# Kernel tuning notes

Hardware: AMD Instinct MI355X
Metric: run time of the kernel (lower is better)

## Reference

```python
import jax, jax.numpy as jnp
import numpy as np

H = 512
W = 512
NSH = 4
MU_BORDER = 1.05
S_MIN = 1.0 / 30.0   # 1 / n_gaussian_max_pixels
S_MAX = 1.0 / 0.75   # 1 / n_gaussian_min_pixels
B = 8192
N = 2048


def setup_inputs() -> dict:
    key = jax.random.key(0)
    k1, k2, k3, k4, k5, k6 = jax.random.split(key, 6)
    x_bx2 = jax.random.uniform(k1, (B, 2), dtype=jnp.float32) * jnp.array([W, H], jnp.float32)
    xyz = jax.random.uniform(k2, (N, 2), dtype=jnp.float32) * 2.0 - 1.0
    features = jax.random.uniform(k3, (N, 2 * NSH + 1, 3), dtype=jnp.float32)
    opacity = 0.1 + 0.9 * jax.random.uniform(k4, (N,), dtype=jnp.float32)
    scaling = jax.random.uniform(k5, (N, 2), dtype=jnp.float32)
    rotation = jax.random.uniform(k6, (N,), dtype=jnp.float32)
    return dict(x_bx2=x_bx2, xyz=xyz, features=features, opacity=opacity,
                scaling=scaling, rotation=rotation)


def reference(x_bx2, xyz, features, opacity, scaling, rotation):
    wh = jnp.array([W, H], x_bx2.dtype)
    xnorm = x_bx2 / wh * 2.0 - 1.0                      # [b,2] in [-1,1]
    mu = jnp.clip(xyz, -1.0, 1.0) * MU_BORDER           # [n,2]
    S = jnp.clip(scaling, 0.0, 1.0) * (S_MAX - S_MIN) + S_MIN   # [n,2]
    ang = jnp.remainder(rotation, 1.0) * (2.0 * jnp.pi)  # [n]
    c = jnp.cos(ang)
    s = jnp.sin(ang)

    # pixel-space offset point - mu: [b,n,2]
    vec = (xnorm[:, None, :] - mu[None, :, :]) * 0.5 * wh
    vx = vec[..., 0]
    vy = vec[..., 1]
    # rotated: R @ v with R = [[c,-s],[s,c]]
    rx = c * vx - s * vy
    ry = s * vx + c * vy
    # scaled Mahalanobis-style squared distance
    d2 = (S[:, 0] * rx) ** 2 + (S[:, 1] * ry) ** 2       # [b,n]
    # validity test done in torch under no_grad: ||S*R*v|| < 5
    valid = jax.lax.stop_gradient(d2) < 25.0

    # unit direction point->gaussian, rotated, then angle for SH basis
    vn = jnp.sqrt(vx * vx + vy * vy)
    inv = 1.0 / (1e-10 + vn)
    nx = vx * inv
    ny = vy * inv
    rnx = c * nx - s * ny
    rny = s * nx + c * ny
    theta = jnp.arctan2(rnx, rny)                        # [b,n] (atan2(rot_x, rot_y) as in torch)

    # SH basis: [1, sin(th), cos(th), sin(2th), cos(2th), ...] -> [b,n,2*NSH+1]
    ks = jnp.arange(1, NSH + 1, dtype=theta.dtype)
    tk = theta[..., None] * ks                           # [b,n,NSH]
    sc = jnp.stack([jnp.sin(tk), jnp.cos(tk)], axis=-1).reshape(*theta.shape, 2 * NSH)
    basis = jnp.concatenate([jnp.ones_like(theta)[..., None], sc], axis=-1)

    rgb = jax.nn.sigmoid(jnp.einsum('bnm,nmc->bnc', basis, features))  # [b,n,3]
    wgt = jnp.exp(-d2) * jnp.clip(opacity, 0.0, 1.0) * valid.astype(rgb.dtype)  # [b,n]
    # accumulate_along_rays == per-ray weighted sum of rgb
    return jnp.einsum('bn,bnc->bc', wgt, rgb)            # [b,3]
```

## Files before the change

### kernel.cpp

```cpp
#include <hip/hip_runtime.h>


constexpr int   BN    = 8192;
constexpr int   NG    = 2048;
constexpr float SMIN  = 1.0f / 30.0f;
constexpr float SSPAN = (1.0f / 0.75f - 1.0f / 30.0f);
constexpr float MUSCALE = 1.05f * 256.0f;
constexpr float LOG2E = 1.44269504088896341f;
constexpr float QT    = 25.0f * 1.44269504088896341f;
constexpr float TWOPI = 6.283185307179586f;
constexpr int   BLOCK = 256;
constexpr int   RC    = 8;
constexpr int   NBLK  = BN / RC;
constexpr int   GPT   = NG / BLOCK;
constexpr int   QMAX  = 2048;

__global__ __launch_bounds__(256) void splat_pre(
    const float* __restrict__ xyz, const float* __restrict__ opac,
    const float* __restrict__ scal, const float* __restrict__ rot,
    float* __restrict__ gp)
{
    const int g = blockIdx.x * 256 + threadIdx.x;
    if (g >= NG) return;
    const float2 xy = reinterpret_cast<const float2*>(xyz)[g];
    const float2 sc = reinterpret_cast<const float2*>(scal)[g];
    const float  rr = rot[g];
    const float  op = fminf(fmaxf(opac[g], 0.0f), 1.0f);
    const float mx = fminf(fmaxf(xy.x, -1.0f), 1.0f) * MUSCALE;
    const float my = fminf(fmaxf(xy.y, -1.0f), 1.0f) * MUSCALE;
    const float s0 = fminf(fmaxf(sc.x, 0.0f), 1.0f) * SSPAN + SMIN;
    const float s1 = fminf(fmaxf(sc.y, 0.0f), 1.0f) * SSPAN + SMIN;
    const float ang = (rr - floorf(rr)) * TWOPI;
    const float cs = cosf(ang);
    const float sn = sinf(ang);
    const float qsx = s0 * s0 * LOG2E;
    const float qsy = s1 * s1 * LOG2E;
    const float c2 = cs * cs, s2 = sn * sn;
    const float A  = fmaf(qsx, c2, qsy * s2);
    const float C  = fmaf(qsx, s2, qsy * c2);
    const float Bq = 2.0f * cs * sn * (qsy - qsx);
    const float l2op = log2f(fmaxf(op, 1e-30f));
    float4* o = reinterpret_cast<float4*>(gp + 8 * g);
    o[0] = make_float4(mx, my, A, Bq);
    o[1] = make_float4(C, l2op, cs, sn);
}

__global__ __launch_bounds__(BLOCK) void splat_main(
    const float* __restrict__ xb,
    const float* __restrict__ gp,
    const float* __restrict__ feat,
    float* __restrict__ out)
{
    __shared__ float    sray[RC * 2];
    __shared__ float    sacc[RC * 3];
    __shared__ unsigned queue[QMAX];
    __shared__ int      qcnt;

    const int tid = threadIdx.x;
    const int rc  = blockIdx.x;

    if (tid == 0) qcnt = 0;
    if (tid < RC) {
        const float2 t = reinterpret_cast<const float2*>(xb)[rc * RC + tid];
        sray[2 * tid + 0] = t.x - 256.0f;
        sray[2 * tid + 1] = t.y - 256.0f;
    }
    if (tid < RC * 3) sacc[tid] = 0.0f;
    __syncthreads();

    float rxs[RC], rys[RC];
    #pragma unroll
    for (int i = 0; i < RC; ++i) { rxs[i] = sray[2 * i]; rys[i] = sray[2 * i + 1]; }

    const float4* __restrict__ gp4 = reinterpret_cast<const float4*>(gp);

    float4 p0 = gp4[2 * tid + 0];
    for (int k = 0; k < GPT; ++k) {
        float4 n0;
        if (k + 1 < GPT) n0 = gp4[2 * ((k + 1) * BLOCK + tid)];
        const float mx = p0.x, my = p0.y, A = p0.z, Bq = p0.w;
        const float C  = gp4[2 * (k * BLOCK + tid) + 1].x;
        const unsigned gbase = (unsigned)(k * BLOCK + tid) << 3;
        #pragma unroll
        for (int i = 0; i < RC; ++i) {
            const float vx = rxs[i] - mx;
            const float vy = rys[i] - my;
            const float q  = fmaf(A, vx * vx, fmaf(Bq, vx * vy, C * (vy * vy)));
            if (q < QT) {
                const int idx = atomicAdd(&qcnt, 1);
                if (idx < QMAX) queue[idx] = gbase | (unsigned)i;
            }
        }
        p0 = n0;
    }
    __syncthreads();

    const int n = min(qcnt, QMAX);
    for (int j = tid; j < n; j += BLOCK) {
        const unsigned e = queue[j];
        const int g = (int)(e >> 3);
        const int i = (int)(e & 7u);

        const float4 a = gp4[2 * g + 0];
        const float4 b = gp4[2 * g + 1];
        const float vx = sray[2 * i + 0] - a.x;
        const float vy = sray[2 * i + 1] - a.y;
        const float q  = fmaf(a.z, vx * vx, fmaf(a.w, vx * vy, b.x * (vy * vy)));
        const float w  = exp2f(b.y - q);
        const float cs = b.z, sn = b.w;
        const float rx = fmaf(cs, vx, -sn * vy);
        const float ry = fmaf(sn, vx,  cs * vy);

        const float iv  = rsqrtf(fmaxf(vx * vx + vy * vy, 1e-24f));
        const float s1v = rx * iv;
        const float c1v = ry * iv;
        const float s2v = 2.0f * s1v * c1v;
        const float c2v = fmaf(-2.0f * s1v, s1v, 1.0f);
        const float s3v = fmaf(s1v, c2v, c1v * s2v);
        const float c3v = fmaf(c1v, c2v, -s1v * s2v);
        const float s4v = 2.0f * s2v * c2v;
        const float c4v = fmaf(-2.0f * s2v, s2v, 1.0f);

        const float* __restrict__ fg = feat + (size_t)g * 27;
        float x0 = fg[0], x1 = fg[1], x2 = fg[2];
        x0 = fmaf(s1v, fg[3],  x0); x1 = fmaf(s1v, fg[4],  x1); x2 = fmaf(s1v, fg[5],  x2);
        x0 = fmaf(c1v, fg[6],  x0); x1 = fmaf(c1v, fg[7],  x1); x2 = fmaf(c1v, fg[8],  x2);
        x0 = fmaf(s2v, fg[9],  x0); x1 = fmaf(s2v, fg[10], x1); x2 = fmaf(s2v, fg[11], x2);
        x0 = fmaf(c2v, fg[12], x0); x1 = fmaf(c2v, fg[13], x1); x2 = fmaf(c2v, fg[14], x2);
        x0 = fmaf(s3v, fg[15], x0); x1 = fmaf(s3v, fg[16], x1); x2 = fmaf(s3v, fg[17], x2);
        x0 = fmaf(c3v, fg[18], x0); x1 = fmaf(c3v, fg[19], x1); x2 = fmaf(c3v, fg[20], x2);
        x0 = fmaf(s4v, fg[21], x0); x1 = fmaf(s4v, fg[22], x1); x2 = fmaf(s4v, fg[23], x2);
        x0 = fmaf(c4v, fg[24], x0); x1 = fmaf(c4v, fg[25], x1); x2 = fmaf(c4v, fg[26], x2);

        atomicAdd(&sacc[3 * i + 0], __fdividef(w, 1.0f + exp2f(-x0 * LOG2E)));
        atomicAdd(&sacc[3 * i + 1], __fdividef(w, 1.0f + exp2f(-x1 * LOG2E)));
        atomicAdd(&sacc[3 * i + 2], __fdividef(w, 1.0f + exp2f(-x2 * LOG2E)));
    }
    __syncthreads();

    if (tid < RC * 3)
        out[rc * (RC * 3) + tid] = sacc[tid];
}

extern "C" void kernel_launch(void* const* d_in, const int* in_sizes, int n_in,
                              void* d_out, int out_size, void* d_ws, size_t ws_size,
                              hipStream_t stream) {
    const float* xb   = (const float*)d_in[0];
    const float* xyz  = (const float*)d_in[1];
    const float* feat = (const float*)d_in[2];
    const float* opac = (const float*)d_in[3];
    const float* scal = (const float*)d_in[4];
    const float* rot  = (const float*)d_in[5];
    float* out = (float*)d_out;
    float* gp  = (float*)d_ws;

    splat_pre<<<dim3(NG / 256), dim3(256), 0, stream>>>(xyz, opac, scal, rot, gp);
    splat_main<<<dim3(NBLK), dim3(BLOCK), 0, stream>>>(xb, gp, feat, out);
}
```

Baseline: 18.10 us.

## Split Gaussian params into SoA arrays and halve rays per block

Stores the per-Gaussian parameters as separate arrays: a float4 with mean and two quadratic coefficients, a second float4 with the remaining terms, and a standalone copy of C. The culling loop then reads contiguous float4s plus a scalar instead of strided 32-byte records. Rays per block drop from 8 to 4, which doubles the block count and shrinks the queue. This improves coalescing and parallelism, but each Gaussian parameter is now reloaded twice as many times across blocks.

```diff
diff --git a/kernel.cpp b/kernel.cpp
--- a/kernel.cpp
+++ b/kernel.cpp
@@ -10,15 +10,19 @@
 constexpr float QT    = 25.0f * 1.44269504088896341f;
 constexpr float TWOPI = 6.283185307179586f;
 constexpr int   BLOCK = 256;
-constexpr int   RC    = 8;
+constexpr int   RC    = 4;
 constexpr int   NBLK  = BN / RC;
 constexpr int   GPT   = NG / BLOCK;
-constexpr int   QMAX  = 2048;
+constexpr int   QMAX  = 1024;
+
+constexpr int WS_LT  = 0;
+constexpr int WS_GPB = WS_LT + NG * 4;
+constexpr int WS_C   = WS_GPB + NG * 4;
 
 __global__ __launch_bounds__(256) void splat_pre(
     const float* __restrict__ xyz, const float* __restrict__ opac,
     const float* __restrict__ scal, const float* __restrict__ rot,
-    float* __restrict__ gp)
+    float* __restrict__ ws)
 {
     const int g = blockIdx.x * 256 + threadIdx.x;
     if (g >= NG) return;
@@ -40,14 +44,14 @@
     const float C  = fmaf(qsx, s2, qsy * c2);
     const float Bq = 2.0f * cs * sn * (qsy - qsx);
     const float l2op = log2f(fmaxf(op, 1e-30f));
-    float4* o = reinterpret_cast<float4*>(gp + 8 * g);
-    o[0] = make_float4(mx, my, A, Bq);
-    o[1] = make_float4(C, l2op, cs, sn);
+    reinterpret_cast<float4*>(ws + WS_LT)[g]  = make_float4(mx, my, A, Bq);
+    reinterpret_cast<float4*>(ws + WS_GPB)[g] = make_float4(C, l2op, cs, sn);
+    ws[WS_C + g] = C;
 }
 
 __global__ __launch_bounds__(BLOCK) void splat_main(
     const float* __restrict__ xb,
-    const float* __restrict__ gp,
+    const float* __restrict__ ws,
     const float* __restrict__ feat,
     float* __restrict__ out)
 {
@@ -72,37 +76,42 @@
     #pragma unroll
     for (int i = 0; i < RC; ++i) { rxs[i] = sray[2 * i]; rys[i] = sray[2 * i + 1]; }
 
-    const float4* __restrict__ gp4 = reinterpret_cast<const float4*>(gp);
+    const float4* __restrict__ lt4  = reinterpret_cast<const float4*>(ws + WS_LT);
+    const float4* __restrict__ gpb4 = reinterpret_cast<const float4*>(ws + WS_GPB);
+    const float*  __restrict__ cArr = ws + WS_C;
 
-    float4 p0 = gp4[2 * tid + 0];
+    float4 p0 = lt4[tid];
+    float  c0 = cArr[tid];
     for (int k = 0; k < GPT; ++k) {
-        float4 n0;
-        if (k + 1 < GPT) n0 = gp4[2 * ((k + 1) * BLOCK + tid)];
-        const float mx = p0.x, my = p0.y, A = p0.z, Bq = p0.w;
-        const float C  = gp4[2 * (k * BLOCK + tid) + 1].x;
-        const unsigned gbase = (unsigned)(k * BLOCK + tid) << 3;
+        float4 n0; float nc;
+        if (k + 1 < GPT) {
+            const int gn = (k + 1) * BLOCK + tid;
+            n0 = lt4[gn];
+            nc = cArr[gn];
+        }
+        const unsigned gbase = (unsigned)(k * BLOCK + tid) << 2;
         #pragma unroll
         for (int i = 0; i < RC; ++i) {
-            const float vx = rxs[i] - mx;
-            const float vy = rys[i] - my;
-            const float q  = fmaf(A, vx * vx, fmaf(Bq, vx * vy, C * (vy * vy)));
+            const float vx = rxs[i] - p0.x;
+            const float vy = rys[i] - p0.y;
+            const float q  = fmaf(p0.z, vx * vx, fmaf(p0.w, vx * vy, c0 * (vy * vy)));
             if (q < QT) {
                 const int idx = atomicAdd(&qcnt, 1);
                 if (idx < QMAX) queue[idx] = gbase | (unsigned)i;
             }
         }
-        p0 = n0;
+        p0 = n0; c0 = nc;
     }
     __syncthreads();
 
     const int n = min(qcnt, QMAX);
     for (int j = tid; j < n; j += BLOCK) {
         const unsigned e = queue[j];
-        const int g = (int)(e >> 3);
-        const int i = (int)(e & 7u);
+        const int g = (int)(e >> 2);
+        const int i = (int)(e & 3u);
 
-        const float4 a = gp4[2 * g + 0];
-        const float4 b = gp4[2 * g + 1];
+        const float4 a = lt4[g];
+        const float4 b = gpb4[g];
         const float vx = sray[2 * i + 0] - a.x;
         const float vy = sray[2 * i + 1] - a.y;
         const float q  = fmaf(a.z, vx * vx, fmaf(a.w, vx * vy, b.x * (vy * vy)));
@@ -152,8 +161,8 @@
     const float* scal = (const float*)d_in[4];
     const float* rot  = (const float*)d_in[5];
     float* out = (float*)d_out;
-    float* gp  = (float*)d_ws;
+    float* ws  = (float*)d_ws;
 
-    splat_pre<<<dim3(NG / 256), dim3(256), 0, stream>>>(xyz, opac, scal, rot, gp);
-    splat_main<<<dim3(NBLK), dim3(BLOCK), 0, stream>>>(xb, gp, feat, out);
+    splat_pre<<<dim3(NG / 256), dim3(256), 0, stream>>>(xyz, opac, scal, rot, ws);
+    splat_main<<<dim3(NBLK), dim3(BLOCK), 0, stream>>>(xb, ws, feat, out);
 }
```

After: 17.07 us. 1.06x faster.
